# Optimization experiments

Measured on AMD Instinct MI355X. Metric: run time of the kernel, lower is better.

Reference implementation:

```python
import jax, jax.numpy as jnp
import numpy as np

B, S, H, NH = 32, 512, 768, 12
EC, EU = 4, 4
CAP = 1.0
DH = H // NH
CAPACITY = int(CAP * B / EC)  # Switch-style capacity per common expert


def setup_inputs() -> dict:
    key = jax.random.key(0)
    ks = jax.random.split(key, 10)
    s = 0.02
    E = EC + EU  # experts stacked: [0:EC]=common, [EC:]=unique
    return {
        "hidden_states": jax.random.normal(ks[0], (B, S, H), jnp.float32),
        "attention_mask": jnp.zeros((B, S), jnp.float32),  # additive mask
        "Wq": jax.random.normal(ks[1], (E, H, H), jnp.float32) * s,
        "bq": jnp.zeros((E, H), jnp.float32),
        "Wk": jax.random.normal(ks[2], (E, H, H), jnp.float32) * s,
        "bk": jnp.zeros((E, H), jnp.float32),
        "Wv": jax.random.normal(ks[3], (E, H, H), jnp.float32) * s,
        "bv": jnp.zeros((E, H), jnp.float32),
        "Wo": jax.random.normal(ks[4], (E, H, H), jnp.float32) * s,
        "bo": jnp.zeros((E, H), jnp.float32),
        "Wsc": jax.random.normal(ks[5], (H, EC), jnp.float32) * s,
        "bsc": jnp.zeros((EC,), jnp.float32),
        "Wsu": jax.random.normal(ks[6], (H, EU), jnp.float32) * s,
        "bsu": jnp.zeros((EU,), jnp.float32),
    }


def reference(hidden_states, attention_mask, Wq, bq, Wk, bk, Wv, bv, Wo, bo,
              Wsc, bsc, Wsu, bsu):
    # ---- common routing (per-sequence top-1 over mean-pooled tokens) ----
    h_mean = hidden_states.mean(axis=1)                       # [B,H]
    pc = jax.nn.softmax(h_mean @ Wsc + bsc, axis=-1)          # [B,EC]
    rc = jnp.argmax(pc, axis=-1)                              # [B]
    pc_max = jnp.max(pc, axis=-1)                             # [B]
    # capacity drop: within each expert keep the CAPACITY highest-prob seqs
    order = jnp.argsort(-pc_max)                              # global desc sort
    oh = jax.nn.one_hot(rc[order], EC, dtype=jnp.int32)       # [B,EC]
    rank = jnp.take_along_axis(jnp.cumsum(oh, axis=0), rc[order][:, None], 1)[:, 0]
    kept = jnp.zeros((B,), bool).at[order].set(rank <= CAPACITY)

    # ---- unique routing for dropped sequences (mean is per-sequence, so
    #      computing on the full batch and masking matches torch) ----
    pu = jax.nn.softmax(h_mean @ Wsu + bsu, axis=-1)          # [B,EU]
    ru = jnp.argmax(pu, axis=-1)
    pu_max = jnp.max(pu, axis=-1)

    # per-sequence expert index into stacked [EC+EU] expert params
    eidx = jnp.where(kept, rc, EC + ru)                       # [B]
    # scaling factor p/stop_grad(p): ==1 in fwd, routes grads to the gate
    scale = jnp.where(kept,
                      pc_max / jax.lax.stop_gradient(pc_max),
                      pu_max / jax.lax.stop_gradient(pu_max))

    # ---- gather-dispatch: per-sequence expert weights ----
    Wq_b, Wk_b, Wv_b, Wo_b = Wq[eidx], Wk[eidx], Wv[eidx], Wo[eidx]  # [B,H,H]
    bq_b, bk_b, bv_b, bo_b = bq[eidx], bk[eidx], bv[eidx], bo[eidx]  # [B,H]

    def heads(t):  # [B,S,H] -> [B,NH,S,DH]
        return t.reshape(B, S, NH, DH).transpose(0, 2, 1, 3)

    q = heads(jnp.einsum('bsh,bhd->bsd', hidden_states, Wq_b) + bq_b[:, None, :])
    k = heads(jnp.einsum('bsh,bhd->bsd', hidden_states, Wk_b) + bk_b[:, None, :])
    v = heads(jnp.einsum('bsh,bhd->bsd', hidden_states, Wv_b) + bv_b[:, None, :])

    scores = jnp.einsum('bhsd,bhtd->bhst', q, k) / np.float32(np.sqrt(DH))
    scores = scores + attention_mask[:, None, None, :]        # additive mask
    attn = jax.nn.softmax(scores, axis=-1)
    ctx = jnp.einsum('bhst,bhtd->bhsd', attn, v)
    ctx = ctx.transpose(0, 2, 1, 3).reshape(B, S, H)

    out = jnp.einsum('bsh,bhd->bsd', ctx, Wo_b) + bo_b[:, None, :]
    return out * scale[:, None, None]
```

## Files before the change

kernel.cpp:

```cpp
#include <hip/hip_runtime.h>
#include <hip/hip_bf16.h>

#define B_ 32
#define S_ 512
#define H_ 768
#define NH_ 12
#define DH_ 64
#define EC_ 4
#define CAPN_ 8

using short8  = __attribute__((ext_vector_type(8))) short;
using floatx4 = __attribute__((ext_vector_type(4))) float;
using bf16 = __hip_bfloat16;

__device__ __forceinline__ void gl_lds16(const void* g, void* l) {
  __builtin_amdgcn_global_load_lds(
      (const __attribute__((address_space(1))) unsigned int*)g,
      (__attribute__((address_space(3))) unsigned int*)l, 16, 0, 0);
}

__global__ void k_mean_convert(const float* __restrict__ X, bf16* __restrict__ Xh,
                               float* __restrict__ partial) {
  int idx = blockIdx.x * 256 + threadIdx.x;
  int b = idx / H_, h = idx - b * H_;
  int s0 = blockIdx.y * 64;
  size_t base = ((size_t)b * S_ + s0) * H_ + h;
  float sum = 0.f;
#pragma unroll 8
  for (int s = 0; s < 64; ++s) {
    float v = X[base + (size_t)s * H_];
    Xh[base + (size_t)s * H_] = __float2bfloat16(v);
    sum += v;
  }
  partial[(size_t)blockIdx.y * (B_ * H_) + idx] = sum;
}

__global__ void k_mean_reduce(const float* __restrict__ partial, float* __restrict__ hmean) {
  int idx = blockIdx.x * 256 + threadIdx.x;
  float s = 0.f;
#pragma unroll
  for (int c = 0; c < 8; ++c) s += partial[(size_t)c * (B_ * H_) + idx];
  hmean[idx] = s * (1.f / 512.f);
}

__global__ void k_wt(const float* __restrict__ Wq, const float* __restrict__ Wk,
                     const float* __restrict__ Wv, const float* __restrict__ Wo,
                     bf16* __restrict__ Wt) {
  __shared__ float tile[32][33];
  int z = blockIdx.z;
  const float* Wbase = (z < 8 ? Wq : z < 16 ? Wk : z < 24 ? Wv : Wo) + (size_t)(z & 7) * H_ * H_;
  int k0 = blockIdx.x * 32, n0 = blockIdx.y * 32;
  int tj = threadIdx.x & 31, ti = threadIdx.x >> 5;
#pragma unroll
  for (int r = 0; r < 4; ++r)
    tile[ti + r * 8][tj] = Wbase[(size_t)(k0 + ti + r * 8) * H_ + n0 + tj];
  __syncthreads();
  bf16* out = Wt + (size_t)z * H_ * H_;
#pragma unroll
  for (int r = 0; r < 4; ++r)
    out[(size_t)(n0 + ti + r * 8) * H_ + k0 + tj] = __float2bfloat16(tile[tj][ti + r * 8]);
}

__global__ void k_gate(const float* __restrict__ hmean,
                       const float* __restrict__ Wsc, const float* __restrict__ bsc,
                       const float* __restrict__ Wsu, const float* __restrict__ bsu,
                       float* __restrict__ logits) {
  int b = blockIdx.x;
  int t = threadIdx.x;
  int g = t >> 3, p = t & 7;
  const float* hm = hmean + (size_t)b * H_;
  const float* w;
  float bias;
  if (g < 4) { w = Wsc + g; bias = bsc[g]; }
  else       { w = Wsu + (g - 4); bias = bsu[g - 4]; }
  float acc = 0.f;
  for (int j = p; j < H_; j += 8) acc += hm[j] * w[j * 4];
  acc += __shfl_xor(acc, 1);
  acc += __shfl_xor(acc, 2);
  acc += __shfl_xor(acc, 4);
  if (p == 0) logits[b * 8 + g] = acc + bias;
}

__global__ void k_route2(const float* __restrict__ logits, int* __restrict__ eidx) {
  __shared__ float pcmax[B_];
  __shared__ int rc_s[B_], ru_s[B_];
  int t = threadIdx.x;
  if (t < B_) {
    float lg[8];
#pragma unroll
    for (int e = 0; e < 8; ++e) lg[e] = logits[t * 8 + e];
    float m = lg[0]; int a = 0;
    for (int e = 1; e < 4; ++e) if (lg[e] > m) { m = lg[e]; a = e; }
    float s = 0.f;
    for (int e = 0; e < 4; ++e) s += expf(lg[e] - m);
    pcmax[t] = 1.f / s;
    rc_s[t] = a;
    float mu = lg[4]; int au = 0;
    for (int e = 1; e < 4; ++e) if (lg[4 + e] > mu) { mu = lg[4 + e]; au = e; }
    ru_s[t] = au;
  }
  __syncthreads();
  if (t == 0) {
    bool used[B_], kept[B_];
    int cnt[EC_] = {0, 0, 0, 0};
    for (int i = 0; i < B_; ++i) used[i] = false;
    for (int i = 0; i < B_; ++i) {
      int best = 0; float bv = -1e30f;
      for (int j = 0; j < B_; ++j)
        if (!used[j] && pcmax[j] > bv) { bv = pcmax[j]; best = j; }
      used[best] = true;
      kept[best] = (++cnt[rc_s[best]] <= CAPN_);
    }
    for (int i = 0; i < B_; ++i)
      eidx[i] = kept[i] ? rc_s[i] : EC_ + ru_s[i];
  }
}

template <int OMODE>
__global__ __launch_bounds__(256) void k_gemm(
    const bf16* __restrict__ A, const bf16* __restrict__ Wt,
    const float* __restrict__ bias0, const float* __restrict__ bias1,
    const float* __restrict__ bias2,
    void* out0, void* out1, void* out2,
    const int* __restrict__ eidx, int mat0) {
  __shared__ __align__(16) char lds[2][32768];
  int bz = blockIdx.z;
  int b = blockIdx.y;
  int e = eidx[b];
  int mtile = blockIdx.x & 3, ntile = blockIdx.x >> 2;
  int m0 = mtile * 128, n0 = ntile * 128;
  const bf16* Ab = A + (size_t)b * S_ * H_;
  const bf16* Wb = Wt + (size_t)((mat0 + bz) * 8 + e) * H_ * H_;
  const float* bias = ((bz == 0) ? bias0 : (bz == 1) ? bias1 : bias2) + (size_t)e * H_;
  void* outp = (bz == 0) ? out0 : (bz == 1) ? out1 : out2;

  int t = threadIdx.x, lane = t & 63, w = t >> 6;
  int wm = (w & 1) * 64, wn = (w >> 1) * 64;
  int lm = lane & 15, lq = lane >> 4;

  auto stage = [&](int kt) {
    char* buf = lds[kt & 1];
#pragma unroll
    for (int r = 0; r < 8; ++r) {
      int c = t + r * 256;
      const bf16* g;
      if (c < 1024) {
        int mm = c >> 3, pos = c & 7, kc = pos ^ (mm & 7);
        g = Ab + (size_t)(m0 + mm) * H_ + kt * 64 + kc * 8;
      } else {
        int c2 = c - 1024;
        int nn = c2 >> 3, pos = c2 & 7, kc = pos ^ (nn & 7);
        g = Wb + (size_t)(n0 + nn) * H_ + kt * 64 + kc * 8;
      }
      gl_lds16(g, buf + (size_t)c * 16);
    }
  };

  floatx4 acc[4][4] = {};
  stage(0);
  __syncthreads();
  for (int kt = 0; kt < 12; ++kt) {
    if (kt < 11) stage(kt + 1);
    const char* cur = lds[kt & 1];
#pragma unroll
    for (int kf = 0; kf < 2; ++kf) {
      int kc = kf * 4 + lq;
      short8 af[4], bf[4];
#pragma unroll
      for (int mf = 0; mf < 4; ++mf) {
        int mm = wm + mf * 16 + lm;
        af[mf] = *(const short8*)(cur + ((size_t)(mm * 8 + (kc ^ (mm & 7)))) * 16);
      }
#pragma unroll
      for (int nf = 0; nf < 4; ++nf) {
        int nn = wn + nf * 16 + lm;
        bf[nf] = *(const short8*)(cur + 16384 + ((size_t)(nn * 8 + (kc ^ (nn & 7)))) * 16);
      }
#pragma unroll
      for (int mf = 0; mf < 4; ++mf)
#pragma unroll
        for (int nf = 0; nf < 4; ++nf)
          acc[mf][nf] = __builtin_amdgcn_mfma_f32_16x16x32_bf16(af[mf], bf[nf], acc[mf][nf], 0, 0, 0);
    }
    if (kt < 11) __syncthreads();
  }
#pragma unroll
  for (int mf = 0; mf < 4; ++mf) {
#pragma unroll
    for (int nf = 0; nf < 4; ++nf) {
      int n = n0 + wn + nf * 16 + lm;
      float bv = bias[n];
      int mrow = m0 + wm + mf * 16 + lq * 4;
      size_t rowbase = ((size_t)b * S_ + mrow) * H_ + n;
#pragma unroll
      for (int r = 0; r < 4; ++r) {
        float v = acc[mf][nf][r] + bv;
        if (OMODE == 0) {
          if (bz == 2) {
            int s = mrow + r;
            ((bf16*)outp)[((size_t)(b * NH_ + (n >> 6))) * 32768 +
                          (size_t)(s >> 3) * 512 + (n & 63) * 8 + (s & 7)] =
                __float2bfloat16(v);
          } else {
            ((bf16*)outp)[rowbase + (size_t)r * H_] = __float2bfloat16(v);
          }
        } else {
          ((float*)outp)[rowbase + (size_t)r * H_] = v;
        }
      }
    }
  }
}

__global__ __launch_bounds__(256, 3) void k_attn(
    const bf16* __restrict__ Q, const bf16* __restrict__ K,
    const bf16* __restrict__ Vt, const float* __restrict__ mask,
    bf16* __restrict__ Ctx) {
  __shared__ __align__(16) bf16 ldsP[4][32 * 72];

  int h = blockIdx.y, b = blockIdx.z;
  int t = threadIdx.x, lane = t & 63, w = t >> 6;
  int lm = lane & 15, lq = lane >> 4;
  int q0 = blockIdx.x * 128 + w * 32;

  short8 qf[2][2];
#pragma unroll
  for (int mf = 0; mf < 2; ++mf)
#pragma unroll
    for (int kf = 0; kf < 2; ++kf)
      qf[mf][kf] = *(const short8*)(Q + ((size_t)(b * S_ + q0 + mf * 16 + lm)) * H_ +
                                    h * DH_ + kf * 32 + lq * 8);

  const bf16* vtb = Vt + ((size_t)(b * NH_ + h)) * 32768;
  bf16* myP = ldsP[w];

  floatx4 oacc[2][4] = {};
  float m_[2][4], l_[2][4];
#pragma unroll
  for (int mf = 0; mf < 2; ++mf)
#pragma unroll
    for (int r = 0; r < 4; ++r) { m_[mf][r] = -1e30f; l_[mf][r] = 0.f; }

  for (int kt = 0; kt < 8; ++kt) {
    floatx4 s[2][4] = {};
    float mv4[4];
#pragma unroll
    for (int nf = 0; nf < 4; ++nf)
      mv4[nf] = mask[(size_t)b * S_ + kt * 64 + nf * 16 + lm];
#pragma unroll
    for (int kf = 0; kf < 2; ++kf) {
      short8 kb4[4];
#pragma unroll
      for (int nf = 0; nf < 4; ++nf)
        kb4[nf] = *(const short8*)(K + ((size_t)(b * S_ + kt * 64 + nf * 16 + lm)) * H_ +
                                   h * DH_ + kf * 32 + lq * 8);
#pragma unroll
      for (int mf = 0; mf < 2; ++mf)
#pragma unroll
        for (int nf = 0; nf < 4; ++nf)
          s[mf][nf] = __builtin_amdgcn_mfma_f32_16x16x32_bf16(qf[mf][kf], kb4[nf], s[mf][nf], 0, 0, 0);
    }
#pragma unroll
    for (int mf = 0; mf < 2; ++mf) {
#pragma unroll
      for (int r = 0; r < 4; ++r) {
#pragma unroll
        for (int nf = 0; nf < 4; ++nf)
          s[mf][nf][r] = s[mf][nf][r] * 0.125f + mv4[nf];
        float tm = fmaxf(fmaxf(s[mf][0][r], s[mf][1][r]), fmaxf(s[mf][2][r], s[mf][3][r]));
        tm = fmaxf(tm, __shfl_xor(tm, 1));
        tm = fmaxf(tm, __shfl_xor(tm, 2));
        tm = fmaxf(tm, __shfl_xor(tm, 4));
        tm = fmaxf(tm, __shfl_xor(tm, 8));
        float mn = fmaxf(m_[mf][r], tm);
        float a = __expf(m_[mf][r] - mn);
        m_[mf][r] = mn;
        int row = mf * 16 + lq * 4 + r;
        float ps = 0.f;
#pragma unroll
        for (int nf = 0; nf < 4; ++nf) {
          float p = __expf(s[mf][nf][r] - mn);
          ps += p;
          int col = (nf * 16 + lm) ^ (lq << 3);
          myP[row * 72 + col] = __float2bfloat16(p);
        }
        ps += __shfl_xor(ps, 1);
        ps += __shfl_xor(ps, 2);
        ps += __shfl_xor(ps, 4);
        ps += __shfl_xor(ps, 8);
        l_[mf][r] = l_[mf][r] * a + ps;
#pragma unroll
        for (int nf = 0; nf < 4; ++nf) oacc[mf][nf][r] *= a;
      }
    }
#pragma unroll
    for (int kf = 0; kf < 2; ++kf) {
      short8 pf[2];
#pragma unroll
      for (int mf = 0; mf < 2; ++mf) {
        int row = mf * 16 + lm;
        int ksw = (kf * 32 + lq * 8) ^ ((((row >> 2) & 3)) << 3);
        pf[mf] = *(const short8*)&myP[row * 72 + ksw];
      }
      short8 vf4[4];
#pragma unroll
      for (int nf = 0; nf < 4; ++nf)
        vf4[nf] = *(const short8*)(vtb + ((size_t)(kt * 8 + kf * 4 + lq)) * 512 +
                                   (nf * 16 + lm) * 8);
#pragma unroll
      for (int mf = 0; mf < 2; ++mf)
#pragma unroll
        for (int nf = 0; nf < 4; ++nf)
          oacc[mf][nf] = __builtin_amdgcn_mfma_f32_16x16x32_bf16(pf[mf], vf4[nf], oacc[mf][nf], 0, 0, 0);
    }
  }
#pragma unroll
  for (int mf = 0; mf < 2; ++mf) {
#pragma unroll
    for (int r = 0; r < 4; ++r) {
      float inv = 1.f / l_[mf][r];
      int row = q0 + mf * 16 + lq * 4 + r;
#pragma unroll
      for (int nf = 0; nf < 4; ++nf)
        Ctx[((size_t)(b * S_ + row)) * H_ + h * DH_ + nf * 16 + lm] =
            __float2bfloat16(oacc[mf][nf][r] * inv);
    }
  }
}

extern "C" void kernel_launch(void* const* d_in, const int* in_sizes, int n_in,
                              void* d_out, int out_size, void* d_ws, size_t ws_size,
                              hipStream_t stream) {
  const float* X    = (const float*)d_in[0];
  const float* mask = (const float*)d_in[1];
  const float* Wq   = (const float*)d_in[2];
  const float* bq   = (const float*)d_in[3];
  const float* Wk   = (const float*)d_in[4];
  const float* bk   = (const float*)d_in[5];
  const float* Wv   = (const float*)d_in[6];
  const float* bv   = (const float*)d_in[7];
  const float* Wo   = (const float*)d_in[8];
  const float* bo   = (const float*)d_in[9];
  const float* Wsc  = (const float*)d_in[10];
  const float* bsc  = (const float*)d_in[11];
  const float* Wsu  = (const float*)d_in[12];
  const float* bsu  = (const float*)d_in[13];

  char* ws = (char*)d_ws;
  int*   eidx    = (int*)ws;
  float* logits  = (float*)(ws + 128);
  float* partial = (float*)(ws + 1280);
  float* hmean   = (float*)(ws + 787712);
  bf16*  Xh      = (bf16*)(ws + 886016);
  bf16*  Wt      = (bf16*)(ws + 26051840);
  bf16*  qb      = (bf16*)(ws + 63800576);
  bf16*  kb      = (bf16*)(ws + 88966400);
  bf16*  Vt      = (bf16*)(ws + 114132224);
  bf16*  ctx     = Xh;

  k_mean_convert<<<dim3(96, 8), 256, 0, stream>>>(X, Xh, partial);
  k_mean_reduce<<<96, 256, 0, stream>>>(partial, hmean);
  k_wt<<<dim3(24, 24, 32), 256, 0, stream>>>(Wq, Wk, Wv, Wo, Wt);
  k_gate<<<B_, 64, 0, stream>>>(hmean, Wsc, bsc, Wsu, bsu, logits);
  k_route2<<<1, 64, 0, stream>>>(logits, eidx);
  k_gemm<0><<<dim3(24, 32, 3), 256, 0, stream>>>(Xh, Wt, bq, bk, bv,
                                                 (void*)qb, (void*)kb, (void*)Vt, eidx, 0);
  k_attn<<<dim3(4, NH_, B_), 256, 0, stream>>>(qb, kb, Vt, mask, ctx);
  k_gemm<1><<<dim3(24, 32, 1), 256, 0, stream>>>(ctx, Wt, bo, bo, bo,
                                                 d_out, d_out, d_out, eidx, 3);
}
```

Measured before the change: 497.5 us.

## Compute transposed attention scores to keep P in registers and drop LDS

The attention kernel now computes S^T (K as the A operand), with K rows permuted so that each lane's accumulator layout matches the B-operand layout the PV MFMA needs. Probabilities are packed into bf16 registers directly and the LDS staging round trip for P is removed, along with the per-row shuffle reductions. Row max and sum now need only two cross-lane shuffles. The mask is read as vector loads, output stores are packed, and the grid is reordered so query tiles of the same head are spread along y. This adds register pressure and depends on the permuted K row mapping being correct.

```diff
diff --git a/kernel.cpp b/kernel.cpp
--- a/kernel.cpp
+++ b/kernel.cpp
@@ -11,12 +11,20 @@
 
 using short8  = __attribute__((ext_vector_type(8))) short;
 using floatx4 = __attribute__((ext_vector_type(4))) float;
+using uint2v  = __attribute__((ext_vector_type(2))) unsigned;
 using bf16 = __hip_bfloat16;
 
 __device__ __forceinline__ void gl_lds16(const void* g, void* l) {
   __builtin_amdgcn_global_load_lds(
       (const __attribute__((address_space(1))) unsigned int*)g,
       (__attribute__((address_space(3))) unsigned int*)l, 16, 0, 0);
+}
+
+__device__ __forceinline__ unsigned pk2(float lo, float hi) {
+  __hip_bfloat162 h = __float22bfloat162_rn(make_float2(lo, hi));
+  unsigned r;
+  __builtin_memcpy(&r, &h, 4);
+  return r;
 }
 
 __global__ void k_mean_convert(const float* __restrict__ X, bf16* __restrict__ Xh,
@@ -216,12 +224,11 @@
     const bf16* __restrict__ Q, const bf16* __restrict__ K,
     const bf16* __restrict__ Vt, const float* __restrict__ mask,
     bf16* __restrict__ Ctx) {
-  __shared__ __align__(16) bf16 ldsP[4][32 * 72];
-
-  int h = blockIdx.y, b = blockIdx.z;
+  int bh = blockIdx.x;
+  int b = bh / NH_, h = bh - b * NH_;
   int t = threadIdx.x, lane = t & 63, w = t >> 6;
   int lm = lane & 15, lq = lane >> 4;
-  int q0 = blockIdx.x * 128 + w * 32;
+  int q0 = blockIdx.y * 128 + w * 32;
 
   short8 qf[2][2];
 #pragma unroll
@@ -231,99 +238,97 @@
       qf[mf][kf] = *(const short8*)(Q + ((size_t)(b * S_ + q0 + mf * 16 + lm)) * H_ +
                                     h * DH_ + kf * 32 + lq * 8);
 
+  int kr = ((lm >> 2) << 3) + (lm & 3);
+  const int koff[4] = {0, 4, 32, 36};
+  const bf16* kbase = K + ((size_t)(b * S_) + kr) * H_ + h * DH_ + lq * 8;
   const bf16* vtb = Vt + ((size_t)(b * NH_ + h)) * 32768;
-  bf16* myP = ldsP[w];
+  const float* mbase = mask + (size_t)b * S_ + lq * 8;
 
   floatx4 oacc[2][4] = {};
-  float m_[2][4], l_[2][4];
-#pragma unroll
-  for (int mf = 0; mf < 2; ++mf)
-#pragma unroll
-    for (int r = 0; r < 4; ++r) { m_[mf][r] = -1e30f; l_[mf][r] = 0.f; }
+  float m_[2] = {-1e30f, -1e30f}, l_[2] = {0.f, 0.f};
 
   for (int kt = 0; kt < 8; ++kt) {
-    floatx4 s[2][4] = {};
-    float mv4[4];
-#pragma unroll
-    for (int nf = 0; nf < 4; ++nf)
-      mv4[nf] = mask[(size_t)b * S_ + kt * 64 + nf * 16 + lm];
+    floatx4 sT[2][4] = {};
 #pragma unroll
     for (int kf = 0; kf < 2; ++kf) {
       short8 kb4[4];
 #pragma unroll
       for (int nf = 0; nf < 4; ++nf)
-        kb4[nf] = *(const short8*)(K + ((size_t)(b * S_ + kt * 64 + nf * 16 + lm)) * H_ +
-                                   h * DH_ + kf * 32 + lq * 8);
+        kb4[nf] = *(const short8*)(kbase + (size_t)(kt * 64 + koff[nf]) * H_ + kf * 32);
 #pragma unroll
       for (int mf = 0; mf < 2; ++mf)
 #pragma unroll
         for (int nf = 0; nf < 4; ++nf)
-          s[mf][nf] = __builtin_amdgcn_mfma_f32_16x16x32_bf16(qf[mf][kf], kb4[nf], s[mf][nf], 0, 0, 0);
-    }
+          sT[mf][nf] = __builtin_amdgcn_mfma_f32_16x16x32_bf16(kb4[nf], qf[mf][kf], sT[mf][nf], 0, 0, 0);
+    }
+    short8 vf[2][4];
+#pragma unroll
+    for (int kf = 0; kf < 2; ++kf)
+#pragma unroll
+      for (int nf = 0; nf < 4; ++nf)
+        vf[kf][nf] = *(const short8*)(vtb + (size_t)(kt * 8 + kf * 4 + lq) * 512 +
+                                      (nf * 16 + lm) * 8);
+    const floatx4* mp = (const floatx4*)(mbase + kt * 64);
+    floatx4 mv[4] = {mp[0], mp[1], mp[8], mp[9]};
+
+    short8 pf[2][2];
 #pragma unroll
     for (int mf = 0; mf < 2; ++mf) {
-#pragma unroll
-      for (int r = 0; r < 4; ++r) {
+      float p[4][4];
+#pragma unroll
+      for (int nf = 0; nf < 4; ++nf)
+#pragma unroll
+        for (int r = 0; r < 4; ++r)
+          p[nf][r] = sT[mf][nf][r] * 0.125f + mv[nf][r];
+      float t01 = fmaxf(fmaxf(fmaxf(p[0][0], p[0][1]), fmaxf(p[0][2], p[0][3])),
+                        fmaxf(fmaxf(p[1][0], p[1][1]), fmaxf(p[1][2], p[1][3])));
+      float t23 = fmaxf(fmaxf(fmaxf(p[2][0], p[2][1]), fmaxf(p[2][2], p[2][3])),
+                        fmaxf(fmaxf(p[3][0], p[3][1]), fmaxf(p[3][2], p[3][3])));
+      float tm = fmaxf(t01, t23);
+      tm = fmaxf(tm, __shfl_xor(tm, 16));
+      tm = fmaxf(tm, __shfl_xor(tm, 32));
+      float mn = fmaxf(m_[mf], tm);
+      float a = __expf(m_[mf] - mn);
+      m_[mf] = mn;
+      float ps = 0.f;
+#pragma unroll
+      for (int nf = 0; nf < 4; ++nf)
+#pragma unroll
+        for (int r = 0; r < 4; ++r) {
+          p[nf][r] = __expf(p[nf][r] - mn);
+          ps += p[nf][r];
+        }
+      ps += __shfl_xor(ps, 16);
+      ps += __shfl_xor(ps, 32);
+      l_[mf] = l_[mf] * a + ps;
+#pragma unroll
+      for (int nf = 0; nf < 4; ++nf) oacc[mf][nf] *= a;
+      union { short8 s8; unsigned u[4]; } pku;
+      pku.u[0] = pk2(p[0][0], p[0][1]); pku.u[1] = pk2(p[0][2], p[0][3]);
+      pku.u[2] = pk2(p[1][0], p[1][1]); pku.u[3] = pk2(p[1][2], p[1][3]);
+      pf[mf][0] = pku.s8;
+      pku.u[0] = pk2(p[2][0], p[2][1]); pku.u[1] = pk2(p[2][2], p[2][3]);
+      pku.u[2] = pk2(p[3][0], p[3][1]); pku.u[3] = pk2(p[3][2], p[3][3]);
+      pf[mf][1] = pku.s8;
+    }
+#pragma unroll
+    for (int kf = 0; kf < 2; ++kf)
+#pragma unroll
+      for (int mf = 0; mf < 2; ++mf)
 #pragma unroll
         for (int nf = 0; nf < 4; ++nf)
-          s[mf][nf][r] = s[mf][nf][r] * 0.125f + mv4[nf];
-        float tm = fmaxf(fmaxf(s[mf][0][r], s[mf][1][r]), fmaxf(s[mf][2][r], s[mf][3][r]));
-        tm = fmaxf(tm, __shfl_xor(tm, 1));
-        tm = fmaxf(tm, __shfl_xor(tm, 2));
-        tm = fmaxf(tm, __shfl_xor(tm, 4));
-        tm = fmaxf(tm, __shfl_xor(tm, 8));
-        float mn = fmaxf(m_[mf][r], tm);
-        float a = __expf(m_[mf][r] - mn);
-        m_[mf][r] = mn;
-        int row = mf * 16 + lq * 4 + r;
-        float ps = 0.f;
-#pragma unroll
-        for (int nf = 0; nf < 4; ++nf) {
-          float p = __expf(s[mf][nf][r] - mn);
-          ps += p;
-          int col = (nf * 16 + lm) ^ (lq << 3);
-          myP[row * 72 + col] = __float2bfloat16(p);
-        }
-        ps += __shfl_xor(ps, 1);
-        ps += __shfl_xor(ps, 2);
-        ps += __shfl_xor(ps, 4);
-        ps += __shfl_xor(ps, 8);
-        l_[mf][r] = l_[mf][r] * a + ps;
-#pragma unroll
-        for (int nf = 0; nf < 4; ++nf) oacc[mf][nf][r] *= a;
-      }
-    }
-#pragma unroll
-    for (int kf = 0; kf < 2; ++kf) {
-      short8 pf[2];
-#pragma unroll
-      for (int mf = 0; mf < 2; ++mf) {
-        int row = mf * 16 + lm;
-        int ksw = (kf * 32 + lq * 8) ^ ((((row >> 2) & 3)) << 3);
-        pf[mf] = *(const short8*)&myP[row * 72 + ksw];
-      }
-      short8 vf4[4];
-#pragma unroll
-      for (int nf = 0; nf < 4; ++nf)
-        vf4[nf] = *(const short8*)(vtb + ((size_t)(kt * 8 + kf * 4 + lq)) * 512 +
-                                   (nf * 16 + lm) * 8);
-#pragma unroll
-      for (int mf = 0; mf < 2; ++mf)
-#pragma unroll
-        for (int nf = 0; nf < 4; ++nf)
-          oacc[mf][nf] = __builtin_amdgcn_mfma_f32_16x16x32_bf16(pf[mf], vf4[nf], oacc[mf][nf], 0, 0, 0);
-    }
+          oacc[mf][nf] = __builtin_amdgcn_mfma_f32_16x16x32_bf16(vf[kf][nf], pf[mf][kf], oacc[mf][nf], 0, 0, 0);
   }
 #pragma unroll
   for (int mf = 0; mf < 2; ++mf) {
-#pragma unroll
-    for (int r = 0; r < 4; ++r) {
-      float inv = 1.f / l_[mf][r];
-      int row = q0 + mf * 16 + lq * 4 + r;
-#pragma unroll
-      for (int nf = 0; nf < 4; ++nf)
-        Ctx[((size_t)(b * S_ + row)) * H_ + h * DH_ + nf * 16 + lm] =
-            __float2bfloat16(oacc[mf][nf][r] * inv);
+    float inv = 1.f / l_[mf];
+    bf16* op = Ctx + ((size_t)(b * S_ + q0 + mf * 16 + lm)) * H_ + h * DH_ + lq * 4;
+#pragma unroll
+    for (int nf = 0; nf < 4; ++nf) {
+      uint2v o;
+      o.x = pk2(oacc[mf][nf][0] * inv, oacc[mf][nf][1] * inv);
+      o.y = pk2(oacc[mf][nf][2] * inv, oacc[mf][nf][3] * inv);
+      *(uint2v*)(op + nf * 16) = o;
     }
   }
 }
@@ -365,7 +370,7 @@
   k_route2<<<1, 64, 0, stream>>>(logits, eidx);
   k_gemm<0><<<dim3(24, 32, 3), 256, 0, stream>>>(Xh, Wt, bq, bk, bv,
                                                  (void*)qb, (void*)kb, (void*)Vt, eidx, 0);
-  k_attn<<<dim3(4, NH_, B_), 256, 0, stream>>>(qb, kb, Vt, mask, ctx);
+  k_attn<<<dim3(B_ * NH_, 4), 256, 0, stream>>>(qb, kb, Vt, mask, ctx);
   k_gemm<1><<<dim3(24, 32, 1), 256, 0, stream>>>(ctx, Wt, bo, bo, bo,
                                                  d_out, d_out, d_out, eidx, 3);
 }
```

After: 475.0 us. -4.5%, faster.
